# Performance work log

Measured on AMD Instinct MI355X. Metric: run time of the kernel, lower is better.

## Reference

```python
import jax, jax.numpy as jnp
import numpy as np

EPS = 1e-5

def _layer_norm(x, w, b):
    mu = jnp.mean(x, axis=-1, keepdims=True)
    var = jnp.mean((x - mu) ** 2, axis=-1, keepdims=True)
    return (x - mu) * jax.lax.rsqrt(var + EPS) * w + b

B, N, C, D = 8, 16384, 256, 2
K = 4096  # ceil(N / 4)

def setup_inputs() -> dict:
    key = jax.random.key(0)
    k0, k1, k2, k3 = jax.random.split(key, 4)
    pos = jax.random.uniform(k0, (B, N, D), dtype=jnp.float32)
    feat = jax.random.normal(k1, (B, N, C), dtype=jnp.float32)
    assignment = jax.random.randint(k2, (B, N), 0, K)
    norm_w = jnp.ones((C + D,), jnp.float32)
    norm_b = jnp.zeros((C + D,), jnp.float32)
    lin_w = jax.random.normal(k3, (2 * C, C + D), jnp.float32) * 0.02
    return {"pos": pos, "feat": feat, "assignment": assignment,
            "norm_w": norm_w, "norm_b": norm_b, "lin_w": lin_w}

def reference(pos, feat, assignment, norm_w, norm_b, lin_w):
    b, n, c = feat.shape
    d = pos.shape[2]
    k = K
    # normalize coordinates by per-dim global max
    pos = pos / jnp.max(pos.reshape(-1, d), axis=0)
    # flatten (batch, cluster) into segments for one big segment_sum
    seg = (assignment + jnp.arange(b, dtype=assignment.dtype)[:, None] * k).reshape(-1)  # [b*n]
    count = jax.ops.segment_sum(jnp.ones((b * n,), pos.dtype), seg,
                                num_segments=b * k).reshape(b, k)
    safe = jnp.maximum(count, 1.0)
    # cluster mean position (scatter_add + divide)
    mean_pos = jax.ops.segment_sum(pos.reshape(-1, d), seg,
                                   num_segments=b * k).reshape(b, k, d) / safe[..., None]
    # relative position via gather
    idx = jnp.broadcast_to(assignment[:, :, None], (b, n, d))
    rel_pos = pos - jnp.take_along_axis(mean_pos, idx, axis=1)
    # norm + linear (dim+pos_dim -> 2*dim, no bias)
    h = _layer_norm(jnp.concatenate([feat, rel_pos], axis=-1), norm_w, norm_b)
    h = jnp.einsum('bnf,of->bno', h, lin_w)  # [b, n, 2c]
    # cluster mean pooling of features (segment sum / count)
    merged = jax.ops.segment_sum(h.reshape(b * n, 2 * c), seg,
                                 num_segments=b * k).reshape(b, k, 2 * c) / safe[..., None]
    # zero out empty clusters and emit validity mask (valid_row_idx path)
    valid = (count > 0).astype(merged.dtype)  # [b, k]
    new_feat = merged * valid[..., None]
    new_pos = mean_pos * valid[..., None]
    new_mask = valid[..., None]  # [b, k, 1]
    return (new_pos, new_feat, new_mask)
```

## Files before the change

kernel.cpp:

```cpp
#include <hip/hip_runtime.h>

#define BB 8
#define NN 16384
#define CC 256
#define KK 4096
#define FDIM 258
#define FP 320
#define OC 512
#define NPTS (BB * NN)
#define NROWS (BB * KK)
#define CAP 64
#define LNEPS 1e-5f

#define OUT_FEAT_OFF 65536
#define OUT_MASK_OFF (65536 + 16777216)

#define OFF_MAX 0
#define OFF_ICOUNT 16
#define MEMSET_FLOATS (16 + NROWS)
#define OFF_ACCH 32784
#define ACC_FSLOTS (NROWS * FP / 2)
#define OFF_INV (OFF_ACCH + ACC_FSLOTS)
#define OFF_LIST (OFF_INV + NROWS)
#define OFF_WPH (OFF_LIST + NROWS * CAP)

typedef _Float16 h8v __attribute__((ext_vector_type(8)));
typedef _Float16 h4v __attribute__((ext_vector_type(4)));
typedef float f4v __attribute__((ext_vector_type(4)));

#define PREP_PB 512
#define PREP_WB 160

__global__ __launch_bounds__(256) void k_prep(const float* __restrict__ pos,
                                              const int* __restrict__ asg,
                                              const float* __restrict__ lw,
                                              float* ws) {
    int bid = blockIdx.x;
    if (bid < PREP_PB) {
        int i = bid * 256 + threadIdx.x;
        int* icount = (int*)(ws + OFF_ICOUNT);
        int* list = (int*)(ws + OFF_LIST);
        float2 p = ((const float2*)pos)[i];
        int b = i >> 14;
        int row = b * KK + asg[i];
        int slot = atomicAdd(icount + row, 1);
        if (slot < CAP) list[row * CAP + slot] = i;
        float mx = p.x, my = p.y;
        for (int off = 32; off > 0; off >>= 1) {
            mx = fmaxf(mx, __shfl_down(mx, off));
            my = fmaxf(my, __shfl_down(my, off));
        }
        if ((threadIdx.x & 63) == 0) {
            atomicMax((int*)(ws + OFF_MAX + 0), __float_as_int(mx));
            atomicMax((int*)(ws + OFF_MAX + 1), __float_as_int(my));
        }
    } else {
        _Float16* Wh = (_Float16*)(ws + OFF_WPH);
        int e = ((bid - PREP_PB) * 256 + threadIdx.x) * 4;
        int o = e / FP, f = e - o * FP;
        h4v h;
#pragma unroll
        for (int u = 0; u < 4; ++u)
            h[u] = (f + u < FDIM) ? (_Float16)lw[o * FDIM + f + u] : (_Float16)0.f;
        *(h4v*)(Wh + e) = h;
    }
}

__global__ __launch_bounds__(256) void k_gather(
    const float* __restrict__ feat, const float* __restrict__ pos,
    const float* __restrict__ nw, const float* __restrict__ nb,
    float* ws, float* __restrict__ out) {
    int t = threadIdx.x;
    int lane = t & 63;
    int row = (blockIdx.x << 2) + (t >> 6);
    const int* icount = (const int*)(ws + OFF_ICOUNT);
    const int* list = (const int*)(ws + OFF_LIST);
    _Float16* Ah = (_Float16*)(ws + OFF_ACCH);

    int cnt = icount[row];
    if (cnt > CAP) cnt = CAP;
    float fcnt = (float)cnt;
    float invc = 1.f / fmaxf(fcnt, 1.f);
    float mxx = ws[OFF_MAX + 0], mxy = ws[OFF_MAX + 1];

    int ptl = (lane < cnt) ? list[row * CAP + lane] : 0;
    float px = 0.f, py = 0.f;
    if (lane < cnt) {
        float2 p = ((const float2*)pos)[ptl];
        px = p.x / mxx;
        py = p.y / mxy;
    }
    float sx = px, sy = py;
    for (int m = 32; m; m >>= 1) {
        sx += __shfl_xor(sx, m);
        sy += __shfl_xor(sy, m);
    }
    float meanx = sx * invc, meany = sy * invc;
    float valid = (cnt > 0) ? 1.f : 0.f;
    if (lane == 0) {
        out[2 * row + 0] = meanx * valid;
        out[2 * row + 1] = meany * valid;
        out[OUT_MASK_OFF + row] = valid;
        ws[OFF_INV + row] = invc;
    }

    float a0 = 0.f, a1 = 0.f, a2 = 0.f, a3 = 0.f, arx = 0.f, ary = 0.f;
    for (int s = 0; s < cnt; ++s) {
        int pt = __shfl(ptl, s);
        float rx = __shfl(px, s) - meanx;
        float ry = __shfl(py, s) - meany;
        float4 v = ((const float4*)(feat + (size_t)pt * CC))[lane];
        float S = v.x + v.y + v.z + v.w;
        float Q = v.x * v.x + v.y * v.y + v.z * v.z + v.w * v.w;
        for (int m = 32; m; m >>= 1) {
            S += __shfl_xor(S, m);
            Q += __shfl_xor(Q, m);
        }
        S += rx + ry;
        Q += rx * rx + ry * ry;
        float mu = S * (1.f / FDIM);
        float var = Q * (1.f / FDIM) - mu * mu;
        float rs = rsqrtf(var + LNEPS);
        a0 += (v.x - mu) * rs;
        a1 += (v.y - mu) * rs;
        a2 += (v.z - mu) * rs;
        a3 += (v.w - mu) * rs;
        arx += (rx - mu) * rs;
        ary += (ry - mu) * rs;
    }
    float4 w4 = ((const float4*)nw)[lane];
    float4 b4 = ((const float4*)nb)[lane];
    h4v h;
    h[0] = (_Float16)(a0 * w4.x + fcnt * b4.x);
    h[1] = (_Float16)(a1 * w4.y + fcnt * b4.y);
    h[2] = (_Float16)(a2 * w4.z + fcnt * b4.z);
    h[3] = (_Float16)(a3 * w4.w + fcnt * b4.w);
    *(h4v*)(Ah + (size_t)row * FP + lane * 4) = h;
    if (lane >= 16 && lane < 32) {
        h4v z = {};
        if (lane == 16) {
            z[0] = (_Float16)(arx * nw[256] + fcnt * nb[256]);
            z[1] = (_Float16)(ary * nw[257] + fcnt * nb[257]);
        }
        *(h4v*)(Ah + (size_t)row * FP + 256 + (lane - 16) * 4) = z;
    }
}

#define GM 128
#define GN 128
#define GK 64

__global__ __launch_bounds__(256) void k_gemm(const float* __restrict__ ws,
                                              float* __restrict__ out) {
    __shared__ _Float16 As[GM][GK];
    __shared__ _Float16 Bs[GN][GK];
    const _Float16* Ah = (const _Float16*)(ws + OFF_ACCH);
    const _Float16* Wh = (const _Float16*)(ws + OFF_WPH);
    const float* inv = ws + OFF_INV;

    int t = threadIdx.x;
    int lane = t & 63;
    int wv = t >> 6;
    int wr = wv & 1, wc = wv >> 1;
    int row0 = blockIdx.x * GM, col0 = blockIdx.y * GN;
    int l15 = lane & 15, kq = lane >> 4;
    int sw = l15 & 7;

    f4v acc[4][4] = {};

    for (int k0 = 0; k0 < FP; k0 += GK) {
#pragma unroll
        for (int l = 0; l < 4; ++l) {
            int c = l * 256 + t;
            int r = c >> 3, ch = c & 7;
            int pc = ch ^ (r & 7);
            *(uint4*)&As[r][pc * 8] = *(const uint4*)(Ah + (size_t)(row0 + r) * FP + k0 + ch * 8);
            *(uint4*)&Bs[r][pc * 8] = *(const uint4*)(Wh + (size_t)(col0 + r) * FP + k0 + ch * 8);
        }
        __syncthreads();
#pragma unroll
        for (int ks = 0; ks < 2; ++ks) {
            h8v af[4], bf[4];
            int lc = ((ks << 2) | kq);
#pragma unroll
            for (int i = 0; i < 4; ++i)
                af[i] = *(const h8v*)&As[wr * 64 + i * 16 + l15][(lc ^ sw) * 8];
#pragma unroll
            for (int j = 0; j < 4; ++j)
                bf[j] = *(const h8v*)&Bs[wc * 64 + j * 16 + l15][(lc ^ sw) * 8];
#pragma unroll
            for (int i = 0; i < 4; ++i)
#pragma unroll
                for (int j = 0; j < 4; ++j)
                    acc[i][j] = __builtin_amdgcn_mfma_f32_16x16x32_f16(
                        af[i], bf[j], acc[i][j], 0, 0, 0);
        }
        __syncthreads();
    }

#pragma unroll
    for (int i = 0; i < 4; ++i) {
#pragma unroll
        for (int r = 0; r < 4; ++r) {
            int row = row0 + wr * 64 + i * 16 + kq * 4 + r;
            float sc = inv[row];
#pragma unroll
            for (int j = 0; j < 4; ++j) {
                int col = col0 + wc * 64 + j * 16 + l15;
                out[OUT_FEAT_OFF + (size_t)row * OC + col] = acc[i][j][r] * sc;
            }
        }
    }
}

extern "C" void kernel_launch(void* const* d_in, const int* in_sizes, int n_in,
                              void* d_out, int out_size, void* d_ws, size_t ws_size,
                              hipStream_t stream) {
    const float* pos = (const float*)d_in[0];
    const float* feat = (const float*)d_in[1];
    const int* asg = (const int*)d_in[2];
    const float* nw = (const float*)d_in[3];
    const float* nb = (const float*)d_in[4];
    const float* lw = (const float*)d_in[5];
    float* out = (float*)d_out;
    float* ws = (float*)d_ws;

    hipMemsetAsync(d_ws, 0, (size_t)MEMSET_FLOATS * sizeof(float), stream);
    k_prep<<<PREP_PB + PREP_WB, 256, 0, stream>>>(pos, asg, lw, ws);
    k_gather<<<NROWS / 4, 256, 0, stream>>>(feat, pos, nw, nb, ws, out);
    k_gemm<<<dim3(NROWS / GM, OC / GN), 256, 0, stream>>>(ws, out);
}
```

Baseline: 311.1 us.

## Process four cluster members per wave in gather and swizzle block-to-XCD mapping

The gather kernel now splits each wave into four 16-lane groups, and each group handles a different cluster member per iteration. This cuts the serial loop trip count and shortens the per-point reduction, at the cost of a final cross-group shuffle merge and more registers. Both the gather and GEMM kernels also remap block indices so that consecutive rows and tiles land on the same XCD, which is meant to improve L2 locality. The GEMM launch grid is flattened to 1D to support the remap.

```diff
diff --git a/kernel.cpp b/kernel.cpp
--- a/kernel.cpp
+++ b/kernel.cpp
@@ -72,7 +72,10 @@
     float* ws, float* __restrict__ out) {
     int t = threadIdx.x;
     int lane = t & 63;
-    int row = (blockIdx.x << 2) + (t >> 6);
+    int bswz = ((blockIdx.x & 7) << 10) + (blockIdx.x >> 3);
+    int row = (bswz << 2) + (t >> 6);
+    int q = lane >> 4;
+    int ll = lane & 15;
     const int* icount = (const int*)(ws + OFF_ICOUNT);
     const int* list = (const int*)(ws + OFF_LIST);
     _Float16* Ah = (_Float16*)(ws + OFF_ACCH);
@@ -104,15 +107,26 @@
         ws[OFF_INV + row] = invc;
     }
 
-    float a0 = 0.f, a1 = 0.f, a2 = 0.f, a3 = 0.f, arx = 0.f, ary = 0.f;
-    for (int s = 0; s < cnt; ++s) {
+    float4 a0 = {0.f, 0.f, 0.f, 0.f}, a1 = {0.f, 0.f, 0.f, 0.f};
+    float4 a2 = {0.f, 0.f, 0.f, 0.f}, a3 = {0.f, 0.f, 0.f, 0.f};
+    float arx = 0.f, ary = 0.f;
+    for (int s0 = 0; s0 < cnt; s0 += 4) {
+        int s = s0 + q;
         int pt = __shfl(ptl, s);
         float rx = __shfl(px, s) - meanx;
         float ry = __shfl(py, s) - meany;
-        float4 v = ((const float4*)(feat + (size_t)pt * CC))[lane];
-        float S = v.x + v.y + v.z + v.w;
-        float Q = v.x * v.x + v.y * v.y + v.z * v.z + v.w * v.w;
-        for (int m = 32; m; m >>= 1) {
+        const float4* fr = (const float4*)(feat + (size_t)pt * CC);
+        float4 v0 = fr[ll];
+        float4 v1 = fr[16 + ll];
+        float4 v2 = fr[32 + ll];
+        float4 v3 = fr[48 + ll];
+        float S = (v0.x + v0.y + v0.z + v0.w) + (v1.x + v1.y + v1.z + v1.w) +
+                  (v2.x + v2.y + v2.z + v2.w) + (v3.x + v3.y + v3.z + v3.w);
+        float Q = v0.x * v0.x + v0.y * v0.y + v0.z * v0.z + v0.w * v0.w +
+                  v1.x * v1.x + v1.y * v1.y + v1.z * v1.z + v1.w * v1.w +
+                  v2.x * v2.x + v2.y * v2.y + v2.z * v2.z + v2.w * v2.w +
+                  v3.x * v3.x + v3.y * v3.y + v3.z * v3.z + v3.w * v3.w;
+        for (int m = 1; m < 16; m <<= 1) {
             S += __shfl_xor(S, m);
             Q += __shfl_xor(Q, m);
         }
@@ -120,21 +134,36 @@
         Q += rx * rx + ry * ry;
         float mu = S * (1.f / FDIM);
         float var = Q * (1.f / FDIM) - mu * mu;
-        float rs = rsqrtf(var + LNEPS);
-        a0 += (v.x - mu) * rs;
-        a1 += (v.y - mu) * rs;
-        a2 += (v.z - mu) * rs;
-        a3 += (v.w - mu) * rs;
-        arx += (rx - mu) * rs;
-        ary += (ry - mu) * rs;
-    }
+        float w = (s < cnt) ? rsqrtf(var + LNEPS) : 0.f;
+        a0.x += (v0.x - mu) * w; a0.y += (v0.y - mu) * w;
+        a0.z += (v0.z - mu) * w; a0.w += (v0.w - mu) * w;
+        a1.x += (v1.x - mu) * w; a1.y += (v1.y - mu) * w;
+        a1.z += (v1.z - mu) * w; a1.w += (v1.w - mu) * w;
+        a2.x += (v2.x - mu) * w; a2.y += (v2.y - mu) * w;
+        a2.z += (v2.z - mu) * w; a2.w += (v2.w - mu) * w;
+        a3.x += (v3.x - mu) * w; a3.y += (v3.y - mu) * w;
+        a3.z += (v3.z - mu) * w; a3.w += (v3.w - mu) * w;
+        arx += (rx - mu) * w;
+        ary += (ry - mu) * w;
+    }
+#define MRG(x)                  \
+    x += __shfl_xor(x, 16);     \
+    x += __shfl_xor(x, 32);
+    MRG(a0.x) MRG(a0.y) MRG(a0.z) MRG(a0.w)
+    MRG(a1.x) MRG(a1.y) MRG(a1.z) MRG(a1.w)
+    MRG(a2.x) MRG(a2.y) MRG(a2.z) MRG(a2.w)
+    MRG(a3.x) MRG(a3.y) MRG(a3.z) MRG(a3.w)
+    MRG(arx) MRG(ary)
+#undef MRG
+
     float4 w4 = ((const float4*)nw)[lane];
     float4 b4 = ((const float4*)nb)[lane];
+    float4 aq = (q == 0) ? a0 : (q == 1) ? a1 : (q == 2) ? a2 : a3;
     h4v h;
-    h[0] = (_Float16)(a0 * w4.x + fcnt * b4.x);
-    h[1] = (_Float16)(a1 * w4.y + fcnt * b4.y);
-    h[2] = (_Float16)(a2 * w4.z + fcnt * b4.z);
-    h[3] = (_Float16)(a3 * w4.w + fcnt * b4.w);
+    h[0] = (_Float16)(aq.x * w4.x + fcnt * b4.x);
+    h[1] = (_Float16)(aq.y * w4.y + fcnt * b4.y);
+    h[2] = (_Float16)(aq.z * w4.z + fcnt * b4.z);
+    h[3] = (_Float16)(aq.w * w4.w + fcnt * b4.w);
     *(h4v*)(Ah + (size_t)row * FP + lane * 4) = h;
     if (lane >= 16 && lane < 32) {
         h4v z = {};
@@ -162,7 +191,11 @@
     int lane = t & 63;
     int wv = t >> 6;
     int wr = wv & 1, wc = wv >> 1;
-    int row0 = blockIdx.x * GM, col0 = blockIdx.y * GN;
+    int wg = blockIdx.x;
+    int idx = wg >> 3;
+    int rowtile = ((wg & 7) << 5) + (idx >> 2);
+    int row0 = rowtile * GM;
+    int col0 = (idx & 3) * GN;
     int l15 = lane & 15, kq = lane >> 4;
     int sw = l15 & 7;
 
@@ -228,5 +261,5 @@
     hipMemsetAsync(d_ws, 0, (size_t)MEMSET_FLOATS * sizeof(float), stream);
     k_prep<<<PREP_PB + PREP_WB, 256, 0, stream>>>(pos, asg, lw, ws);
     k_gather<<<NROWS / 4, 256, 0, stream>>>(feat, pos, nw, nb, ws, out);
-    k_gemm<<<dim3(NROWS / GM, OC / GN), 256, 0, stream>>>(ws, out);
-}
+    k_gemm<<<NROWS / GM * (OC / GN), 256, 0, stream>>>(ws, out);
+}
```

New measurement: 307.4 us. About the same (-1.2%).
